# Optimization experiments

Measured on AMD Instinct MI355X. Metric: run time of the kernel, lower is better.

## Reference

```python
import jax, jax.numpy as jnp
import numpy as np

N = 10000        # num nodes
E = 160000       # num edges (before self-loops)
D = 128          # input_dim == 4*hidden_dim
H = 4            # heads for first 19 layers
C = 32           # hidden_dim (per-head channels)
L_MID = 19       # layers with relu (convs[0..18]); last layer is heads=1, concat=False
NEG_SLOPE = 0.2  # PyG GATConv default negative_slope
EPS = 1e-16      # PyG softmax epsilon


def setup_inputs() -> dict:
    key = jax.random.key(0)
    ks = jax.random.split(key, 10)
    s = 0.1  # keep activations stable across 20 layers
    x = jax.random.normal(ks[0], (N, D), jnp.float32)
    edge_index = jax.random.randint(ks[1], (2, E), 0, N, dtype=jnp.int64)
    Ws = jax.random.normal(ks[2], (L_MID, D, H * C), jnp.float32) * s
    a_src = jax.random.normal(ks[3], (L_MID, H, C), jnp.float32) * s
    a_dst = jax.random.normal(ks[4], (L_MID, H, C), jnp.float32) * s
    bs = jnp.zeros((L_MID, H * C), jnp.float32)
    W_last = jax.random.normal(ks[5], (D, D), jnp.float32) * s
    a_src_last = jax.random.normal(ks[6], (1, D), jnp.float32) * s
    a_dst_last = jax.random.normal(ks[7], (1, D), jnp.float32) * s
    b_last = jnp.zeros((D,), jnp.float32)
    return {"x": x, "edge_index": edge_index, "Ws": Ws, "a_src": a_src,
            "a_dst": a_dst, "bs": bs, "W_last": W_last,
            "a_src_last": a_src_last, "a_dst_last": a_dst_last, "b_last": b_last}


def _gat_layer(x, src, dst, W, asrc, adst, heads, ch):
    # x: [N, Din]; W: [Din, heads*ch]; asrc/adst: [heads, ch]
    h = (x @ W).reshape(N, heads, ch)                       # [N,H,C]
    es = jnp.einsum('nhc,hc->nh', h, asrc)                  # [N,H]
    ed = jnp.einsum('nhc,hc->nh', h, adst)                  # [N,H]
    e = jax.nn.leaky_relu(es[src] + ed[dst], NEG_SLOPE)     # [Etot,H]
    # segment softmax over incoming edges of each dst node
    m = jax.ops.segment_max(e, dst, num_segments=N)         # [N,H]
    p = jnp.exp(e - m[dst])
    z = jax.ops.segment_sum(p, dst, num_segments=N)         # [N,H]
    alpha = p / (z[dst] + EPS)                              # [Etot,H]
    msg = h[src] * alpha[:, :, None]                        # [Etot,H,C]
    return jax.ops.segment_sum(msg, dst, num_segments=N)    # [N,H,C]


def reference(x, edge_index, Ws, a_src, a_dst, bs, W_last, a_src_last, a_dst_last, b_last):
    # PyG GATConv adds self-loops by default
    loop = jnp.arange(N, dtype=edge_index.dtype)
    src = jnp.concatenate([edge_index[0], loop])
    dst = jnp.concatenate([edge_index[1], loop])

    def mid_step(h, params):
        W, asrc, adst, b = params
        out = _gat_layer(h, src, dst, W, asrc, adst, H, C).reshape(N, H * C) + b
        return jax.nn.relu(out), None  # training dropout omitted (eval mode)

    x, _ = jax.lax.scan(mid_step, x, (Ws, a_src, a_dst, bs))
    # final layer: heads=1, concat=False -> mean over heads, no relu
    out = _gat_layer(x, src, dst, W_last, a_src_last, a_dst_last, 1, D)
    return out.mean(axis=1) + b_last
```

## Files before the change

kernel.cpp:

```cpp
#include <hip/hip_runtime.h>
#include <hip/hip_bf16.h>
#include <hip/hip_fp16.h>
#include <math.h>

#define D 128
#define NEG 0.2f
#define EPSV 1e-16f
#define NPB 8
#define GRP_N 4
#define CAP 64


template<int HNEXT>
__device__ __forceinline__ void gemv_phase(const float (*rbuf)[D], int nbase, int N,
                                           const float* __restrict__ Wn,
                                           const float* __restrict__ av_, const float* __restrict__ bv_,
                                           unsigned short* __restrict__ h_out, float* __restrict__ es_out,
                                           float* __restrict__ ed_out, float (*pE)[2], float (*pD)[2]){
  const int t   = threadIdx.x;
  const int col = t & (D-1);
  const int g   = t >> 7;
  const float av = av_[col], bv = bv_[col];
  const float* __restrict__ r[GRP_N];
  #pragma unroll
  for (int j=0;j<GRP_N;j++) r[j] = rbuf[g*GRP_N + j];
  float acc[GRP_N];
  #pragma unroll
  for (int j=0;j<GRP_N;j++) acc[j]=0.f;

  #pragma unroll 4
  for (int k=0;k<D;k+=4){
    const float w0 = Wn[(size_t)(k+0)*D + col];
    const float w1 = Wn[(size_t)(k+1)*D + col];
    const float w2 = Wn[(size_t)(k+2)*D + col];
    const float w3 = Wn[(size_t)(k+3)*D + col];
    #pragma unroll
    for (int j=0;j<GRP_N;j++){
      const float4 xv = *reinterpret_cast<const float4*>(r[j] + k);
      acc[j] = fmaf(xv.w, w3, fmaf(xv.z, w2, fmaf(xv.y, w1, fmaf(xv.x, w0, acc[j]))));
    }
  }

  if constexpr (HNEXT==4){
    #pragma unroll
    for (int j=0;j<GRP_N;j++){
      const int n = nbase + g*GRP_N + j;
      if (n < N){
        const unsigned short hu = __half_as_ushort(__float2half_rn(acc[j]));
        __builtin_nontemporal_store(hu, &h_out[(size_t)n*D + col]);
        float ps = acc[j]*av, pd = acc[j]*bv;
        #pragma unroll
        for (int off=16; off; off>>=1){ ps += __shfl_xor(ps, off, 32); pd += __shfl_xor(pd, off, 32); }
        if ((col&31)==0){ es_out[n*4 + (col>>5)] = ps; ed_out[n*4 + (col>>5)] = pd; }
      }
    }
  } else {
    const int half = (t>>6)&1;
    #pragma unroll
    for (int j=0;j<GRP_N;j++){
      const int n = nbase + g*GRP_N + j;
      float ps = 0.f, pd = 0.f;
      if (n < N){
        const unsigned short hu = __half_as_ushort(__float2half_rn(acc[j]));
        __builtin_nontemporal_store(hu, &h_out[(size_t)n*D + col]);
        ps = acc[j]*av; pd = acc[j]*bv;
      }
      #pragma unroll
      for (int off=32; off; off>>=1){ ps += __shfl_xor(ps, off, 64); pd += __shfl_xor(pd, off, 64); }
      if ((t&63)==0){ pE[g*GRP_N+j][half]=ps; pD[g*GRP_N+j][half]=pd; }
    }
    __syncthreads();
    if (t < NPB){
      const int n = nbase + t;
      if (n < N){
        es_out[n] = pE[t][0]+pE[t][1];
        ed_out[n] = pD[t][0]+pD[t][1];
      }
    }
  }
}

__launch_bounds__(256, 4)
__global__ void linear0_kernel(const float* __restrict__ x, const float* __restrict__ Wn,
                               const float* __restrict__ an_src, const float* __restrict__ an_dst,
                               int N, int E, const int* __restrict__ esrc, const int* __restrict__ edst,
                               int* __restrict__ deg, int* __restrict__ csr_src,
                               unsigned short* __restrict__ h_out, float* __restrict__ es_out, float* __restrict__ ed_out){
  __shared__ float rbuf[NPB][D];
  __shared__ float pE[NPB][2], pD[NPB][2];
  const int t = threadIdx.x;
  const int nbase = blockIdx.x*NPB;
  {
    const int gid = blockIdx.x*256 + t;
    const int gs  = gridDim.x*256;
    const int tot = E + N;
    for (int i = gid; i < tot; i += gs){
      int s2, d2;
      if (i < E){ s2 = esrc[i]; d2 = edst[i]; } else { s2 = i - E; d2 = i - E; }
      const int pos = atomicAdd(&deg[d2], 1);
      if (pos < CAP) csr_src[d2*CAP + pos] = s2;
    }
  }
  {
    const int row = t >> 5;
    const int cc  = (t & 31) * 4;
    int n = nbase + row; if (n > N-1) n = N-1;
    const float4 v = *reinterpret_cast<const float4*>(x + (size_t)n*D + cc);
    *reinterpret_cast<float4*>(&rbuf[row][cc]) = v;
  }
  __syncthreads();
  gemv_phase<4>(rbuf, nbase, N, Wn, an_src, an_dst, h_out, es_out, ed_out, pE, pD);
}

template<int HNEXT>
__launch_bounds__(256, 4)
__global__ void fused_kernel(const unsigned short* __restrict__ h, const float* __restrict__ es, const float* __restrict__ ed,
                             const int* __restrict__ deg, const int* __restrict__ csr_src,
                             const float* __restrict__ bias,
                             const float* __restrict__ Wn, const float* __restrict__ an_src, const float* __restrict__ an_dst,
                             int N, unsigned short* __restrict__ h_out, float* __restrict__ es_out, float* __restrict__ ed_out){
  __shared__ int   sIdx[NPB][32];
  __shared__ float sP[NPB][32][4];
  __shared__ float rbuf[NPB][D];
  __shared__ float pE[NPB][2], pD[NPB][2];
  const int t = threadIdx.x;
  const int hw  = t >> 5;
  const int l32 = t & 31;
  const int cq   = l32 * 4;
  const int myh4 = l32 >> 3;
  const int nbase = blockIdx.x*NPB;
  const int n = nbase + hw;

  if (n < N){
    const int start = n*CAP;
    const int end   = start + min(deg[n], CAP);
    const float4 edv = *reinterpret_cast<const float4*>(ed + (size_t)n*4);
    float4 a0 = make_float4(0.f,0.f,0.f,0.f);
    float4 a1 = make_float4(0.f,0.f,0.f,0.f);
    float z0 = 0.f, z1 = 0.f;

    for (int t0 = start; t0 < end; t0 += 32){
      const int cnt = min(32, end - t0);
      {
        int sOff = 0; float p0=0.f,p1=0.f,p2=0.f,p3=0.f;
        if (l32 < cnt){
          const int s = csr_src[t0 + l32];
          sOff = s*D;
          const float4 e4 = *reinterpret_cast<const float4*>(es + (size_t)s*4);
          float q0 = e4.x + edv.x; q0 = (q0>=0.f)? q0 : NEG*q0; q0 = fminf(q0, 80.f);
          float q1 = e4.y + edv.y; q1 = (q1>=0.f)? q1 : NEG*q1; q1 = fminf(q1, 80.f);
          float q2 = e4.z + edv.z; q2 = (q2>=0.f)? q2 : NEG*q2; q2 = fminf(q2, 80.f);
          float q3 = e4.w + edv.w; q3 = (q3>=0.f)? q3 : NEG*q3; q3 = fminf(q3, 80.f);
          p0 = __expf(q0); p1 = __expf(q1); p2 = __expf(q2); p3 = __expf(q3);
        }
        sIdx[hw][l32] = sOff;
        *reinterpret_cast<float4*>(&sP[hw][l32][0]) = make_float4(p0,p1,p2,p3);
      }
      int e = 0;
      #pragma unroll 4
      for (; e+2 <= cnt; e += 2){
        const int   off0 = sIdx[hw][e];
        const int   off1 = sIdx[hw][e+1];
        const float p0   = sP[hw][e][myh4];
        const float p1   = sP[hw][e+1][myh4];
        union { uint2 u; __half2 h2[2]; } c0, c1;
        c0.u = *reinterpret_cast<const uint2*>(h + (size_t)off0 + cq);
        c1.u = *reinterpret_cast<const uint2*>(h + (size_t)off1 + cq);
        const float2 f0a = __half22float2(c0.h2[0]);
        const float2 f0b = __half22float2(c0.h2[1]);
        const float2 f1a = __half22float2(c1.h2[0]);
        const float2 f1b = __half22float2(c1.h2[1]);
        z0 += p0; z1 += p1;
        a0.x = fmaf(p0, f0a.x, a0.x); a1.x = fmaf(p1, f1a.x, a1.x);
        a0.y = fmaf(p0, f0a.y, a0.y); a1.y = fmaf(p1, f1a.y, a1.y);
        a0.z = fmaf(p0, f0b.x, a0.z); a1.z = fmaf(p1, f1b.x, a1.z);
        a0.w = fmaf(p0, f0b.y, a0.w); a1.w = fmaf(p1, f1b.y, a1.w);
      }
      if (e < cnt){
        const int   off = sIdx[hw][e];
        const float p   = sP[hw][e][myh4];
        union { uint2 u; __half2 h2[2]; } c0;
        c0.u = *reinterpret_cast<const uint2*>(h + (size_t)off + cq);
        const float2 fa = __half22float2(c0.h2[0]);
        const float2 fb = __half22float2(c0.h2[1]);
        z0 += p;
        a0.x = fmaf(p, fa.x, a0.x);
        a0.y = fmaf(p, fa.y, a0.y);
        a0.z = fmaf(p, fb.x, a0.z);
        a0.w = fmaf(p, fb.y, a0.w);
      }
    }
    const float z = z0 + z1;
    const float4 acc = make_float4(a0.x+a1.x, a0.y+a1.y, a0.z+a1.z, a0.w+a1.w);
    const float inv = 1.f/(z + EPSV);
    const float4 bv = *reinterpret_cast<const float4*>(bias + cq);
    float4 o;
    o.x = fmaxf(fmaf(acc.x, inv, bv.x), 0.f);
    o.y = fmaxf(fmaf(acc.y, inv, bv.y), 0.f);
    o.z = fmaxf(fmaf(acc.z, inv, bv.z), 0.f);
    o.w = fmaxf(fmaf(acc.w, inv, bv.w), 0.f);
    *reinterpret_cast<float4*>(&rbuf[hw][cq]) = o;
  } else {
    *reinterpret_cast<float4*>(&rbuf[hw][cq]) = make_float4(0.f,0.f,0.f,0.f);
  }
  __syncthreads();
  gemv_phase<HNEXT>(rbuf, nbase, N, Wn, an_src, an_dst, h_out, es_out, ed_out, pE, pD);
}

__launch_bounds__(256, 4)
__global__ void final_agg_kernel(const unsigned short* __restrict__ h, const float* __restrict__ es, const float* __restrict__ ed,
                                 const int* __restrict__ deg, const int* __restrict__ csr_src,
                                 const float* __restrict__ bias, float* __restrict__ out, int N){
  __shared__ int   sIdx[NPB][32];
  __shared__ float sP[NPB][32];
  const int t = threadIdx.x;
  const int hw  = t >> 5;
  const int l32 = t & 31;
  const int cq  = l32 * 4;
  const int n = blockIdx.x*NPB + hw;
  if (n >= N) return;
  const int start = n*CAP;
  const int end   = start + min(deg[n], CAP);
  const float edn = ed[n];
  float4 acc = make_float4(0.f,0.f,0.f,0.f);
  float z = 0.f;
  for (int t0 = start; t0 < end; t0 += 32){
    const int cnt = min(32, end - t0);
    {
      int sOff = 0; float p0 = 0.f;
      if (l32 < cnt){
        const int s = csr_src[t0 + l32];
        sOff = s*D;
        float q0 = es[s] + edn; q0 = (q0>=0.f)? q0 : NEG*q0; q0 = fminf(q0, 80.f);
        p0 = __expf(q0);
      }
      sIdx[hw][l32] = sOff;
      sP[hw][l32] = p0;
    }
    #pragma unroll 8
    for (int e = 0; e < cnt; e++){
      const int   off = sIdx[hw][e];
      const float p   = sP[hw][e];
      union { uint2 u; __half2 h2[2]; } c0;
      c0.u = *reinterpret_cast<const uint2*>(h + (size_t)off + cq);
      const float2 fa = __half22float2(c0.h2[0]);
      const float2 fb = __half22float2(c0.h2[1]);
      z += p;
      acc.x = fmaf(p, fa.x, acc.x);
      acc.y = fmaf(p, fa.y, acc.y);
      acc.z = fmaf(p, fb.x, acc.z);
      acc.w = fmaf(p, fb.y, acc.w);
    }
  }
  const float inv = 1.f/(z + EPSV);
  const float4 bv = *reinterpret_cast<const float4*>(bias + cq);
  float4 o;
  o.x = fmaf(acc.x, inv, bv.x);
  o.y = fmaf(acc.y, inv, bv.y);
  o.z = fmaf(acc.z, inv, bv.z);
  o.w = fmaf(acc.w, inv, bv.w);
  *reinterpret_cast<float4*>(&out[(size_t)n*D + cq]) = o;
}

extern "C" void kernel_launch(void* const* d_in, const int* in_sizes, int n_in,
                              void* d_out, int out_size, void* d_ws, size_t ws_size,
                              hipStream_t stream) {
  const float* x          = (const float*)d_in[0];
  const int*   ei         = (const int*)d_in[1];
  const float* Ws         = (const float*)d_in[2];
  const float* a_src      = (const float*)d_in[3];
  const float* a_dst      = (const float*)d_in[4];
  const float* bs         = (const float*)d_in[5];
  const float* W_last     = (const float*)d_in[6];
  const float* a_src_last = (const float*)d_in[7];
  const float* a_dst_last = (const float*)d_in[8];
  const float* b_last     = (const float*)d_in[9];

  const int N = in_sizes[0]/D;
  const int E = in_sizes[1]/2;
  const int L = in_sizes[2]/(D*D);
  const int* esrc = ei;
  const int* edst = ei + E;

  char* ws = (char*)d_ws;
  unsigned short* h0 = (unsigned short*)ws;  ws += (size_t)N*D*sizeof(unsigned short);
  unsigned short* h1 = (unsigned short*)ws;  ws += (size_t)N*D*sizeof(unsigned short);
  float* es0 = (float*)ws;  ws += (size_t)N*4*sizeof(float);
  float* es1 = (float*)ws;  ws += (size_t)N*4*sizeof(float);
  float* ed0 = (float*)ws;  ws += (size_t)N*4*sizeof(float);
  float* ed1 = (float*)ws;  ws += (size_t)N*4*sizeof(float);
  int* deg     = (int*)ws;  ws += (size_t)N*sizeof(int);
  int* csr_src = (int*)ws;  ws += (size_t)N*CAP*sizeof(int);

  const int gA = (N + NPB - 1)/NPB;

  hipMemsetAsync(deg, 0, (size_t)N*sizeof(int), stream);
  linear0_kernel<<<gA, 256, 0, stream>>>(x, Ws, a_src, a_dst, N, E, esrc, edst,
                                         deg, csr_src, h0, es0, ed0);

  const unsigned short *hc = h0;
  const float *esc = es0, *edc = ed0;
  unsigned short *hn = h1;
  float *esn = es1, *edn = ed1;

  for (int l = 0; l < L-1; l++){
    fused_kernel<4><<<gA, 256, 0, stream>>>(hc, esc, edc, deg, csr_src,
                                            bs + (size_t)l*D,
                                            Ws + (size_t)(l+1)*D*D, a_src + (size_t)(l+1)*D, a_dst + (size_t)(l+1)*D,
                                            N, hn, esn, edn);
    const unsigned short* th = hc; hc = hn; hn = (unsigned short*)th;
    const float* tf;
    tf = esc; esc = esn; esn = (float*)tf;
    tf = edc; edc = edn; edn = (float*)tf;
  }

  fused_kernel<1><<<gA, 256, 0, stream>>>(hc, esc, edc, deg, csr_src,
                                          bs + (size_t)(L-1)*D,
                                          W_last, a_src_last, a_dst_last,
                                          N, hn, esn, edn);
  {
    const unsigned short* th = hc; hc = hn; hn = (unsigned short*)th;
    const float* tf;
    tf = esc; esc = esn; esn = (float*)tf;
    tf = edc; edc = edn; edn = (float*)tf;
  }

  final_agg_kernel<<<gA, 256, 0, stream>>>(hc, esc, edc, deg, csr_src, b_last, (float*)d_out, N);
}
```

Before: 364.5 us.

## Pre-convert layer weights to packed half2 and raise occupancy bound to 8

Adds a kernel that converts all layer weight matrices (including the last) into fp16 pairs interleaved along the k dimension, and the GEMV phase reads half2 and widens to float. This halves the weight bytes read per block from L2, which every block re-reads for every node group. Launch bounds also go from 4 to 8 blocks per SM to allow more concurrent waves. The cost is fp16 rounding of the weights, an extra conversion launch on each call, and register pressure from the tighter launch bound.

```diff
diff --git a/kernel.cpp b/kernel.cpp
--- a/kernel.cpp
+++ b/kernel.cpp
@@ -9,11 +9,28 @@
 #define NPB 8
 #define GRP_N 4
 #define CAP 64
-
+#define WH_PER ((D/2)*D)
+
+
+__launch_bounds__(256, 8)
+__global__ void wconvert_kernel(const float* __restrict__ Ws, const float* __restrict__ W_last,
+                                int L, __half2* __restrict__ Wh){
+  const int i = blockIdx.x*blockDim.x + threadIdx.x;
+  const int tot = (L+1)*WH_PER;
+  if (i >= tot) return;
+  const int l  = i / WH_PER;
+  const int r  = i % WH_PER;
+  const int kk = r / D;
+  const int col = r % D;
+  const float* W = (l < L) ? (Ws + (size_t)l*D*D) : W_last;
+  const float w0 = W[(size_t)(2*kk)*D + col];
+  const float w1 = W[(size_t)(2*kk+1)*D + col];
+  Wh[i] = __floats2half2_rn(w0, w1);
+}
 
 template<int HNEXT>
 __device__ __forceinline__ void gemv_phase(const float (*rbuf)[D], int nbase, int N,
-                                           const float* __restrict__ Wn,
+                                           const __half2* __restrict__ Wn2,
                                            const float* __restrict__ av_, const float* __restrict__ bv_,
                                            unsigned short* __restrict__ h_out, float* __restrict__ es_out,
                                            float* __restrict__ ed_out, float (*pE)[2], float (*pD)[2]){
@@ -30,14 +47,14 @@
 
   #pragma unroll 4
   for (int k=0;k<D;k+=4){
-    const float w0 = Wn[(size_t)(k+0)*D + col];
-    const float w1 = Wn[(size_t)(k+1)*D + col];
-    const float w2 = Wn[(size_t)(k+2)*D + col];
-    const float w3 = Wn[(size_t)(k+3)*D + col];
+    const __half2 wh0 = Wn2[(size_t)(k>>1)*D + col];
+    const __half2 wh1 = Wn2[(size_t)((k>>1)+1)*D + col];
+    const float2 w01 = __half22float2(wh0);
+    const float2 w23 = __half22float2(wh1);
     #pragma unroll
     for (int j=0;j<GRP_N;j++){
       const float4 xv = *reinterpret_cast<const float4*>(r[j] + k);
-      acc[j] = fmaf(xv.w, w3, fmaf(xv.z, w2, fmaf(xv.y, w1, fmaf(xv.x, w0, acc[j]))));
+      acc[j] = fmaf(xv.w, w23.y, fmaf(xv.z, w23.x, fmaf(xv.y, w01.y, fmaf(xv.x, w01.x, acc[j]))));
     }
   }
 
@@ -80,8 +97,8 @@
   }
 }
 
-__launch_bounds__(256, 4)
-__global__ void linear0_kernel(const float* __restrict__ x, const float* __restrict__ Wn,
+__launch_bounds__(256, 8)
+__global__ void linear0_kernel(const float* __restrict__ x, const __half2* __restrict__ Wh0,
                                const float* __restrict__ an_src, const float* __restrict__ an_dst,
                                int N, int E, const int* __restrict__ esrc, const int* __restrict__ edst,
                                int* __restrict__ deg, int* __restrict__ csr_src,
@@ -109,15 +126,15 @@
     *reinterpret_cast<float4*>(&rbuf[row][cc]) = v;
   }
   __syncthreads();
-  gemv_phase<4>(rbuf, nbase, N, Wn, an_src, an_dst, h_out, es_out, ed_out, pE, pD);
+  gemv_phase<4>(rbuf, nbase, N, Wh0, an_src, an_dst, h_out, es_out, ed_out, pE, pD);
 }
 
 template<int HNEXT>
-__launch_bounds__(256, 4)
+__launch_bounds__(256, 8)
 __global__ void fused_kernel(const unsigned short* __restrict__ h, const float* __restrict__ es, const float* __restrict__ ed,
                              const int* __restrict__ deg, const int* __restrict__ csr_src,
                              const float* __restrict__ bias,
-                             const float* __restrict__ Wn, const float* __restrict__ an_src, const float* __restrict__ an_dst,
+                             const __half2* __restrict__ Wn2, const float* __restrict__ an_src, const float* __restrict__ an_dst,
                              int N, unsigned short* __restrict__ h_out, float* __restrict__ es_out, float* __restrict__ ed_out){
   __shared__ int   sIdx[NPB][32];
   __shared__ float sP[NPB][32][4];
@@ -204,10 +221,10 @@
     *reinterpret_cast<float4*>(&rbuf[hw][cq]) = make_float4(0.f,0.f,0.f,0.f);
   }
   __syncthreads();
-  gemv_phase<HNEXT>(rbuf, nbase, N, Wn, an_src, an_dst, h_out, es_out, ed_out, pE, pD);
-}
-
-__launch_bounds__(256, 4)
+  gemv_phase<HNEXT>(rbuf, nbase, N, Wn2, an_src, an_dst, h_out, es_out, ed_out, pE, pD);
+}
+
+__launch_bounds__(256, 8)
 __global__ void final_agg_kernel(const unsigned short* __restrict__ h, const float* __restrict__ es, const float* __restrict__ ed,
                                  const int* __restrict__ deg, const int* __restrict__ csr_src,
                                  const float* __restrict__ bias, float* __restrict__ out, int N){
@@ -291,11 +308,14 @@
   float* ed1 = (float*)ws;  ws += (size_t)N*4*sizeof(float);
   int* deg     = (int*)ws;  ws += (size_t)N*sizeof(int);
   int* csr_src = (int*)ws;  ws += (size_t)N*CAP*sizeof(int);
+  __half2* Wh  = (__half2*)ws; ws += (size_t)(L+1)*WH_PER*sizeof(__half2);
 
   const int gA = (N + NPB - 1)/NPB;
+  const int gW = ((L+1)*WH_PER + 255)/256;
 
   hipMemsetAsync(deg, 0, (size_t)N*sizeof(int), stream);
-  linear0_kernel<<<gA, 256, 0, stream>>>(x, Ws, a_src, a_dst, N, E, esrc, edst,
+  wconvert_kernel<<<gW, 256, 0, stream>>>(Ws, W_last, L, Wh);
+  linear0_kernel<<<gA, 256, 0, stream>>>(x, Wh, a_src, a_dst, N, E, esrc, edst,
                                          deg, csr_src, h0, es0, ed0);
 
   const unsigned short *hc = h0;
@@ -306,7 +326,7 @@
   for (int l = 0; l < L-1; l++){
     fused_kernel<4><<<gA, 256, 0, stream>>>(hc, esc, edc, deg, csr_src,
                                             bs + (size_t)l*D,
-                                            Ws + (size_t)(l+1)*D*D, a_src + (size_t)(l+1)*D, a_dst + (size_t)(l+1)*D,
+                                            Wh + (size_t)(l+1)*WH_PER, a_src + (size_t)(l+1)*D, a_dst + (size_t)(l+1)*D,
                                             N, hn, esn, edn);
     const unsigned short* th = hc; hc = hn; hn = (unsigned short*)th;
     const float* tf;
@@ -316,7 +336,7 @@
 
   fused_kernel<1><<<gA, 256, 0, stream>>>(hc, esc, edc, deg, csr_src,
                                           bs + (size_t)(L-1)*D,
-                                          W_last, a_src_last, a_dst_last,
+                                          Wh + (size_t)L*WH_PER, a_src_last, a_dst_last,
                                           N, hn, esn, edn);
   {
     const unsigned short* th = hc; hc = hn; hn = (unsigned short*)th;
```

Result: slower. 454.1 us (+24.6%).
